# Kernel tuning notes

Measured on AMD Instinct MI355X. Metric: run time of the kernel, lower is better.

The kernel has to match this reference:

```python
import jax, jax.numpy as jnp
import numpy as np

B, DIM, H, W = 8, 384, 64, 64
HEADS = 8
D = DIM // HEADS            # 48, per-head channel dim
DH = D // 2                 # 24
D2 = D // 3 * 2             # 32, conv_up hidden width (ratio=3)


def setup_inputs() -> dict:
    key = jax.random.key(0)
    ks = jax.random.split(key, 12)
    rn = lambda k, s, sc=0.05: jax.random.normal(k, s, dtype=jnp.float32) * sc
    return {
        "x": rn(ks[0], (B, DIM, H, W), 1.0),
        "w_qkv": rn(ks[1], (3 * DIM, DIM)),          # 1x1 conv dim->3dim, no bias
        "w_dw": rn(ks[2], (3 * DIM, 1, 3, 3)),       # depthwise 3x3, groups=3dim
        "temperature": jnp.ones((HEADS, 1, 1), jnp.float32),
        "w_ar": rn(ks[3], (1, D)),                   # conv_attn_right
        "w_vr": rn(ks[4], (DH, D)),                  # conv_v_right
        "w_up1": rn(ks[5], (D2, DH)),                # conv_up[0]
        "b_up1": jnp.zeros((D2,), jnp.float32),
        "ln_g": jnp.ones((D2, HEADS, 1), jnp.float32),   # LayerNorm([D2, 8, 1])
        "ln_b": jnp.zeros((D2, HEADS, 1), jnp.float32),
        "w_up2": rn(ks[6], (D, D2)),                 # conv_up[3]
        "b_up2": jnp.zeros((D,), jnp.float32),
        "w_al": rn(ks[7], (DH, D)),                  # conv_attn_left
        "w_vl": rn(ks[8], (DH, D)),                  # conv_v_left
        "w_proj": rn(ks[9], (DIM, HEADS)),           # project_out: Conv2d(heads, dim, 1)
    }


def reference(x, w_qkv, w_dw, temperature, w_ar, w_vr, w_up1, b_up1,
              ln_g, ln_b, w_up2, b_up2, w_al, w_vl, w_proj):
    b, c, h, w = x.shape
    hw = h * w
    # qkv = dwconv3x3(conv1x1(x)); the torch module computes this identically in
    # both spatial_pool and channel_pool, so compute once.
    qkv = jnp.einsum('oc,bchw->bohw', w_qkv, x)
    qkv = jax.lax.conv_general_dilated(
        qkv, w_dw, window_strides=(1, 1), padding='SAME',
        feature_group_count=3 * c, dimension_numbers=('NCHW', 'OIHW', 'NCHW'))
    q, k, v = jnp.split(qkv, 3, axis=1)
    hsplit = lambda t: t.reshape(b, HEADS, D, hw)        # 'b (head c) h w -> b head c (h w)'
    q, k, v = hsplit(q), hsplit(k), hsplit(v)
    l2n = lambda t: t / jnp.maximum(jnp.linalg.norm(t, axis=-1, keepdims=True), 1e-12)
    # elementwise q*k attention, temperature-scaled, softmax over spatial (hw)
    attn = jax.nn.softmax(l2n(q) * l2n(k) * temperature, axis=-1)   # [b,heads,D,hw]

    # ---- spatial_pool branch (produces channel gate) ----
    input_x = jnp.einsum('od,bhdn->bhon', w_vr, v)                  # [b,heads,DH,hw]
    cmask = jax.nn.softmax(jnp.einsum('od,bhdn->bhon', w_ar, attn), axis=-1)  # [b,heads,1,hw]
    ctx = jnp.einsum('bhin,bhjn->bhji', cmask, input_x)             # [b,heads,DH,1]
    ctx = ctx.transpose(0, 2, 1, 3)                                 # [b,DH,heads,1]
    t = jnp.einsum('op,bphl->bohl', w_up1, ctx) + b_up1[None, :, None, None]  # [b,D2,8,1]
    mu = t.mean(axis=(1, 2, 3), keepdims=True)
    var = t.var(axis=(1, 2, 3), keepdims=True)
    t = (t - mu) / jnp.sqrt(var + 1e-5) * ln_g[None] + ln_b[None]
    t = jax.nn.relu(t)
    t = jnp.einsum('op,bphl->bohl', w_up2, t) + b_up2[None, :, None, None]    # [b,D,8,1]
    # torch .view(b, head*d, 1, 1) on a [b, d, head, 1] tensor: plain reshape
    mask_ch = jax.nn.sigmoid(t).reshape(b, c, 1, 1)
    out_spatial = x * mask_ch

    # ---- channel_pool branch (produces spatial gate) ----
    g_x = jnp.einsum('od,bhdn->bhon', w_al, attn)                   # [b,heads,DH,hw]
    avg_x = jax.nn.softmax(g_x.mean(axis=-1), axis=-1)              # [b,heads,DH]
    theta_x = jnp.einsum('od,bhdn->bhon', w_vl, v)                  # [b,heads,DH,hw]
    mask_sp = jax.nn.sigmoid(jnp.einsum('bho,bhon->bhn', avg_x, theta_x))
    mask_sp = mask_sp.reshape(b, HEADS, h, w)
    mask_sp = jnp.einsum('oh,bhxy->boxy', w_proj, mask_sp)          # project_out
    out_channel = x * mask_sp

    return out_spatial + out_channel
```

## Files before the change

### kernel.cpp

```cpp
#include <hip/hip_runtime.h>
#include <math.h>
#include <stdint.h>

#define B_     8
#define DIM_   384
#define HEADS_ 8
#define D_     48
#define DH_    24
#define D2_    32
#define HW_    4096
#define IMG    64
#define CH3    1152

typedef __attribute__((ext_vector_type(8))) __bf16   bf16x8;
typedef __attribute__((ext_vector_type(4))) float    f32x4;
typedef __attribute__((ext_vector_type(8))) unsigned short u16x8;

__device__ __forceinline__ float b2f(unsigned short h){
  union { uint32_t u; float f; } v; v.u = ((uint32_t)h) << 16; return v.f;
}
__device__ __forceinline__ unsigned short f2b(float f){
  union { float f; uint32_t u; } v; v.f = f;
  uint32_t r = v.u + 0x7fffu + ((v.u >> 16) & 1u);
  return (unsigned short)(r >> 16);
}

__device__ __forceinline__ float wred_sum(float v){
#pragma unroll
  for (int m = 32; m; m >>= 1) v += __shfl_xor(v, m);
  return v;
}
__device__ __forceinline__ float wred_max(float v){
#pragma unroll
  for (int m = 32; m; m >>= 1) v = fmaxf(v, __shfl_xor(v, m));
  return v;
}
__device__ __forceinline__ float wred_min(float v){
#pragma unroll
  for (int m = 32; m; m >>= 1) v = fminf(v, __shfl_xor(v, m));
  return v;
}
template<int OP>
__device__ __forceinline__ float block_red(float v, float* lds){
  if (OP == 0) v = wred_sum(v);
  else if (OP == 1) v = wred_max(v);
  else v = wred_min(v);
  const int lane = threadIdx.x & 63;
  const int wid  = threadIdx.x >> 6;
  __syncthreads();
  if (lane == 0) lds[wid] = v;
  __syncthreads();
  const int nw = blockDim.x >> 6;
  float r = lds[0];
  for (int i = 1; i < nw; ++i){
    float o = lds[i];
    if (OP == 0) r += o; else if (OP == 1) r = fmaxf(r, o); else r = fminf(r, o);
  }
  return r;
}

__global__ __launch_bounds__(256)
void k_cvtw(const float* __restrict__ w, unsigned short* __restrict__ wb){
  const int i = (blockIdx.x * 256 + threadIdx.x) * 4;
  float4 v = *reinterpret_cast<const float4*>(w + i);
  wb[i+0] = f2b(v.x); wb[i+1] = f2b(v.y); wb[i+2] = f2b(v.z); wb[i+3] = f2b(v.w);
}

__global__ __launch_bounds__(256)
void k_prep(const float* __restrict__ x, unsigned short* __restrict__ xT){
  __shared__ unsigned short Ts[64][66];
  const int t = threadIdx.x;
  const float* xb = x + ((size_t)blockIdx.z * DIM_ + blockIdx.y * 64) * HW_ + blockIdx.x * 64;
#pragma unroll
  for (int rr = 0; rr < 4; ++rr){
    const int r = (t >> 4) + rr * 16;
    const int c = (t & 15) * 4;
    float4 v = *reinterpret_cast<const float4*>(xb + (size_t)r * HW_ + c);
    Ts[r][c+0] = f2b(v.x); Ts[r][c+1] = f2b(v.y); Ts[r][c+2] = f2b(v.z); Ts[r][c+3] = f2b(v.w);
  }
  __syncthreads();
  const int rn = t >> 2, kc = (t & 3) * 16;
  unsigned short* yb = xT + ((size_t)blockIdx.z * HW_ + blockIdx.x * 64 + rn) * DIM_
                          + blockIdx.y * 64 + kc;
  u16x8 o0, o1;
#pragma unroll
  for (int j = 0; j < 8; ++j){ o0[j] = Ts[kc + j][rn]; o1[j] = Ts[kc + 8 + j][rn]; }
  *reinterpret_cast<u16x8*>(yb)     = o0;
  *reinterpret_cast<u16x8*>(yb + 8) = o1;
}

__global__ __launch_bounds__(256, 2)
void k_gemm(const unsigned short* __restrict__ wb, const unsigned short* __restrict__ xT,
            unsigned short* __restrict__ qkv){
  const int b  = blockIdx.z;
  const int m0 = blockIdx.y * 128;
  const int n0 = blockIdx.x * 128;
  __shared__ unsigned short As[128 * 64];
  __shared__ unsigned short Bs[128 * 64];
  const int t = threadIdx.x;
  const int lane = t & 63;
  const int w = t >> 6, wr = w >> 1, wc = w & 1;
  f32x4 acc[4][4];
#pragma unroll
  for (int i = 0; i < 4; ++i)
#pragma unroll
    for (int j = 0; j < 4; ++j) acc[i][j] = (f32x4){0.f,0.f,0.f,0.f};

  const unsigned short* Ag = wb + (size_t)m0 * DIM_;
  const unsigned short* Bg = xT + ((size_t)b * HW_ + n0) * DIM_;

  for (int k0 = 0; k0 < DIM_; k0 += 64){
#pragma unroll
    for (int i = 0; i < 4; ++i){
      const int q = i * 256 + t;
      const int qb = q & ~63;
      const int r = q >> 3, c = q & 7;
      __builtin_amdgcn_global_load_lds(
        (const __attribute__((address_space(1))) void*)(Ag + (size_t)r * DIM_ + k0 + c * 8),
        (__attribute__((address_space(3))) void*)(As + qb * 8), 16, 0, 0);
    }
#pragma unroll
    for (int i = 0; i < 4; ++i){
      const int q = i * 256 + t;
      const int qb = q & ~63;
      const int r = q >> 3, c = q & 7;
      __builtin_amdgcn_global_load_lds(
        (const __attribute__((address_space(1))) void*)(Bg + (size_t)r * DIM_ + k0 + c * 8),
        (__attribute__((address_space(3))) void*)(Bs + qb * 8), 16, 0, 0);
    }
    __syncthreads();
#pragma unroll
    for (int ks = 0; ks < 2; ++ks){
      const int kb = ks * 32 + (lane >> 4) * 8;
      bf16x8 af[4], bfr[4];
#pragma unroll
      for (int mi = 0; mi < 4; ++mi){
        const int row = wr * 64 + mi * 16 + (lane & 15);
        af[mi] = *reinterpret_cast<const bf16x8*>(As + row * 64 + kb);
      }
#pragma unroll
      for (int ni = 0; ni < 4; ++ni){
        const int row = wc * 64 + ni * 16 + (lane & 15);
        bfr[ni] = *reinterpret_cast<const bf16x8*>(Bs + row * 64 + kb);
      }
#pragma unroll
      for (int mi = 0; mi < 4; ++mi)
#pragma unroll
        for (int ni = 0; ni < 4; ++ni)
          acc[mi][ni] = __builtin_amdgcn_mfma_f32_16x16x32_bf16(af[mi], bfr[ni], acc[mi][ni], 0, 0, 0);
    }
    __syncthreads();
  }
  unsigned short* yb = qkv + ((size_t)b * CH3 + m0) * HW_ + n0;
#pragma unroll
  for (int mi = 0; mi < 4; ++mi){
    const int rbase = wr * 64 + mi * 16 + (lane >> 4) * 4;
#pragma unroll
    for (int ni = 0; ni < 4; ++ni){
      const int col = wc * 64 + ni * 16 + (lane & 15);
#pragma unroll
      for (int r = 0; r < 4; ++r)
        yb[(size_t)(rbase + r) * HW_ + col] = f2b(acc[mi][ni][r]);
    }
  }
}

__global__ __launch_bounds__(256)
void k_dwconv(unsigned short* __restrict__ qkv, const float* __restrict__ w_dw){
  const int pc = blockIdx.x;
  const int ch = pc % CH3;
  unsigned short* plane = qkv + (size_t)pc * HW_;
  const int t  = threadIdx.x;
  const int y  = t >> 2;
  const int x0 = (t & 3) * 16;
  float w9[9];
#pragma unroll
  for (int i = 0; i < 9; ++i) w9[i] = w_dw[ch * 9 + i];
  float acc16[16];
#pragma unroll
  for (int j = 0; j < 16; ++j) acc16[j] = 0.f;
#pragma unroll
  for (int dy = -1; dy <= 1; ++dy){
    const int yy = y + dy;
    if ((unsigned)yy >= (unsigned)IMG) continue;
    const unsigned short* rp = plane + yy * IMG;
    u16x8 C0 = *reinterpret_cast<const u16x8*>(rp + x0);
    u16x8 C1 = *reinterpret_cast<const u16x8*>(rp + x0 + 8);
    float rw[18];
    rw[0]  = (x0 > 0)  ? b2f(rp[x0 - 1])  : 0.f;
    rw[17] = (x0 < 48) ? b2f(rp[x0 + 16]) : 0.f;
#pragma unroll
    for (int j = 0; j < 8; ++j){ rw[1+j] = b2f(C0[j]); rw[9+j] = b2f(C1[j]); }
    const float w0 = w9[(dy+1)*3], w1 = w9[(dy+1)*3+1], w2 = w9[(dy+1)*3+2];
#pragma unroll
    for (int j = 0; j < 16; ++j)
      acc16[j] = fmaf(rw[j], w0, fmaf(rw[j+1], w1, fmaf(rw[j+2], w2, acc16[j])));
  }
  __syncthreads();
  u16x8 o0, o1;
#pragma unroll
  for (int j = 0; j < 8; ++j){ o0[j] = f2b(acc16[j]); o1[j] = f2b(acc16[8+j]); }
  *reinterpret_cast<u16x8*>(plane + (size_t)y * IMG + x0)     = o0;
  *reinterpret_cast<u16x8*>(plane + (size_t)y * IMG + x0 + 8) = o1;
}

__global__ __launch_bounds__(256)
void k_rowstats(const unsigned short* __restrict__ dqkv, const float* __restrict__ temperature,
                const float* __restrict__ w_ar, float* __restrict__ prm){
  const int bid  = blockIdx.x;
  const int d    = bid % D_;
  const int head = (bid / D_) % HEADS_;
  const int b    = bid / (D_ * HEADS_);
  const int cq   = head * D_ + d;
  const unsigned short* qp = dqkv + ((size_t)b * CH3 + cq) * HW_;
  const unsigned short* kp = qp + (size_t)DIM_ * HW_;
  __shared__ float lds[8];
  const int t = threadIdx.x;
  float p[16];
  float sq = 0.f, sk = 0.f, pmx = -3.0e38f, pmn = 3.0e38f;
  {
    u16x8 q0 = *reinterpret_cast<const u16x8*>(qp + t * 16);
    u16x8 q1 = *reinterpret_cast<const u16x8*>(qp + t * 16 + 8);
    u16x8 k0 = *reinterpret_cast<const u16x8*>(kp + t * 16);
    u16x8 k1 = *reinterpret_cast<const u16x8*>(kp + t * 16 + 8);
#pragma unroll
    for (int j = 0; j < 8; ++j){
      float fq = b2f(q0[j]), fk = b2f(k0[j]);
      sq = fmaf(fq, fq, sq); sk = fmaf(fk, fk, sk);
      p[j] = fq * fk; pmx = fmaxf(pmx, p[j]); pmn = fminf(pmn, p[j]);
    }
#pragma unroll
    for (int j = 0; j < 8; ++j){
      float fq = b2f(q1[j]), fk = b2f(k1[j]);
      sq = fmaf(fq, fq, sq); sk = fmaf(fk, fk, sk);
      p[8+j] = fq * fk; pmx = fmaxf(pmx, p[8+j]); pmn = fminf(pmn, p[8+j]);
    }
  }
  sq  = block_red<0>(sq, lds);
  sk  = block_red<0>(sk, lds);
  pmx = block_red<1>(pmx, lds);
  pmn = block_red<2>(pmn, lds);
  const float nq = fmaxf(sqrtf(sq), 1e-12f);
  const float nk = fmaxf(sqrtf(sk), 1e-12f);
  const float c  = temperature[head] / (nq * nk);
  const float m  = (c >= 0.f) ? c * pmx : c * pmn;
  float se = 0.f;
#pragma unroll
  for (int j = 0; j < 16; ++j) se += expf(fmaf(c, p[j], -m));
  se = block_red<0>(se, lds);
  if (t == 0){
    prm[bid*3+0] = c;
    prm[bid*3+1] = m;
    prm[bid*3+2] = w_ar[d] / se;
  }
}

__global__ __launch_bounds__(256)
void k_attn_a(const unsigned short* __restrict__ dqkv, const float* __restrict__ prm,
              float* __restrict__ abuf){
  const int bh   = blockIdx.y;
  const int head = bh & 7, b = bh >> 3;
  const int t = threadIdx.x;
  const int px0 = (blockIdx.x * 256 + t) * 2;
  __shared__ float pc[D_ * 3];
  for (int i = t; i < D_ * 3; i += 256) pc[i] = prm[bh * (D_ * 3) + i];
  __syncthreads();
  const unsigned short* qb = dqkv + ((size_t)b * CH3 + head * D_) * HW_ + px0;
  const unsigned short* kb = qb + (size_t)DIM_ * HW_;
  float a0 = 0.f, a1 = 0.f;
  for (int d = 0; d < D_; ++d){
    const uint32_t qv = *reinterpret_cast<const uint32_t*>(qb + (size_t)d * HW_);
    const uint32_t kv = *reinterpret_cast<const uint32_t*>(kb + (size_t)d * HW_);
    const float cc = pc[d*3], mm = pc[d*3+1], ww = pc[d*3+2];
    const float p0 = b2f((unsigned short)qv) * b2f((unsigned short)kv);
    const float p1 = b2f((unsigned short)(qv >> 16)) * b2f((unsigned short)(kv >> 16));
    a0 = fmaf(ww, expf(fmaf(cc, p0, -mm)), a0);
    a1 = fmaf(ww, expf(fmaf(cc, p1, -mm)), a1);
  }
  float2 o; o.x = a0; o.y = a1;
  *reinterpret_cast<float2*>(abuf + (size_t)bh * HW_ + px0) = o;
}

__global__ __launch_bounds__(256)
void k_cmask(float* __restrict__ abuf){
  const int bh = blockIdx.x;
  float* a = abuf + (size_t)bh * HW_;
  __shared__ float lds[8];
  const int t = threadIdx.x;
  float va[16];
  float mx = -3.0e38f;
#pragma unroll
  for (int i = 0; i < 16; ++i){ va[i] = a[t + i*256]; mx = fmaxf(mx, va[i]); }
  mx = block_red<1>(mx, lds);
  float s = 0.f;
#pragma unroll
  for (int i = 0; i < 16; ++i){ va[i] = expf(va[i]-mx); s += va[i]; }
  s = block_red<0>(s, lds);
  const float inv = 1.f / s;
#pragma unroll
  for (int i = 0; i < 16; ++i) a[t + i*256] = va[i]*inv;
}

__global__ __launch_bounds__(256)
void k_vctx(const unsigned short* __restrict__ dqkv, const float* __restrict__ abuf,
            float* __restrict__ vctx){
  const int bid  = blockIdx.x;
  const int d    = bid % D_;
  const int head = (bid / D_) % HEADS_;
  const int b    = bid / (D_ * HEADS_);
  const unsigned short* vp = dqkv + ((size_t)b * CH3 + 2*DIM_ + head*D_ + d) * HW_;
  const float* cm = abuf + ((size_t)(b * HEADS_ + head)) * HW_;
  __shared__ float lds[8];
  const int t = threadIdx.x;
  float s = 0.f;
  u16x8 v0 = *reinterpret_cast<const u16x8*>(vp + t * 16);
  u16x8 v1 = *reinterpret_cast<const u16x8*>(vp + t * 16 + 8);
#pragma unroll
  for (int j = 0; j < 8; ++j) s = fmaf(cm[t*16 + j],     b2f(v0[j]), s);
#pragma unroll
  for (int j = 0; j < 8; ++j) s = fmaf(cm[t*16 + 8 + j], b2f(v1[j]), s);
  s = block_red<0>(s, lds);
  if (t == 0) vctx[bid] = s;
}

__global__ __launch_bounds__(256)
void k_spmask(const unsigned short* __restrict__ dqkv, const float* __restrict__ w_al,
              const float* __restrict__ w_vl, float* __restrict__ spb){
  const int bh   = blockIdx.y;
  const int head = bh & 7, b = bh >> 3;
  const int t = threadIdx.x;
  const int px0 = (blockIdx.x * 256 + t) * 2;
  __shared__ float u[D_];
  __shared__ float avg[DH_];
  if (t < DH_){
    float s = 0.f;
    for (int d = 0; d < D_; ++d) s += w_al[t*D_ + d];
    avg[t] = s * (1.f/(float)HW_);
  }
  __syncthreads();
  if (t == 0){
    float mx = avg[0];
    for (int o = 1; o < DH_; ++o) mx = fmaxf(mx, avg[o]);
    float s = 0.f;
    for (int o = 0; o < DH_; ++o){ avg[o] = expf(avg[o]-mx); s += avg[o]; }
    const float inv = 1.f/s;
    for (int o = 0; o < DH_; ++o) avg[o] *= inv;
  }
  __syncthreads();
  if (t < D_){
    float s = 0.f;
    for (int o = 0; o < DH_; ++o) s = fmaf(avg[o], w_vl[o*D_ + t], s);
    u[t] = s;
  }
  __syncthreads();
  const unsigned short* vb = dqkv + ((size_t)b * CH3 + 2*DIM_ + head*D_) * HW_ + px0;
  float a0 = 0.f, a1 = 0.f;
  for (int d = 0; d < D_; ++d){
    const uint32_t vv = *reinterpret_cast<const uint32_t*>(vb + (size_t)d * HW_);
    const float ud = u[d];
    a0 = fmaf(ud, b2f((unsigned short)vv), a0);
    a1 = fmaf(ud, b2f((unsigned short)(vv >> 16)), a1);
  }
  float2 o;
  o.x = 1.f/(1.f + expf(-a0));
  o.y = 1.f/(1.f + expf(-a1));
  *reinterpret_cast<float2*>(spb + (size_t)bh * HW_ + px0) = o;
}

__global__ __launch_bounds__(256)
void k_maskch(const float* __restrict__ vctx, const float* __restrict__ w_vr,
              const float* __restrict__ w_up1, const float* __restrict__ b_up1,
              const float* __restrict__ ln_g, const float* __restrict__ ln_b,
              const float* __restrict__ w_up2, const float* __restrict__ b_up2,
              float* __restrict__ mch){
  const int b = blockIdx.x;
  const int t = threadIdx.x;
  __shared__ float vc[HEADS_*D_];
  __shared__ float cx[HEADS_*DH_];
  __shared__ float t1[D2_*HEADS_];
  __shared__ float lds[8];
  for (int i = t; i < HEADS_*D_; i += 256) vc[i] = vctx[b*HEADS_*D_ + i];
  __syncthreads();
  if (t < HEADS_*DH_){
    const int head = t / DH_, o = t % DH_;
    float s = 0.f;
    for (int d = 0; d < D_; ++d) s = fmaf(w_vr[o*D_+d], vc[head*D_+d], s);
    cx[head*DH_+o] = s;
  }
  __syncthreads();
  const int o2 = t >> 3, hh = t & 7;
  float val = b_up1[o2];
  for (int o = 0; o < DH_; ++o) val = fmaf(w_up1[o2*DH_+o], cx[hh*DH_+o], val);
  const float mu  = block_red<0>(val, lds) * (1.f/256.f);
  const float dv  = val - mu;
  const float var = block_red<0>(dv*dv, lds) * (1.f/256.f);
  float yv = dv / sqrtf(var + 1e-5f);
  yv = fmaf(yv, ln_g[t], ln_b[t]);
  yv = fmaxf(yv, 0.f);
  t1[t] = yv;
  __syncthreads();
  for (int idx = t; idx < D_*HEADS_; idx += 256){
    const int d = idx >> 3, head2 = idx & 7;
    float s = b_up2[d];
    for (int o = 0; o < D2_; ++o) s = fmaf(w_up2[d*D2_+o], t1[o*HEADS_+head2], s);
    mch[b*DIM_ + idx] = 1.f/(1.f + expf(-s));
  }
}

__global__ __launch_bounds__(256)
void k_out(const float* __restrict__ x, const float* __restrict__ spb,
           const float* __restrict__ mch, const float* __restrict__ w_proj,
           float* __restrict__ out){
  const int b  = blockIdx.z;
  const int c0 = blockIdx.y * 16;
  const int n  = blockIdx.x * 1024 + threadIdx.x * 4;
  float4 sv[8];
#pragma unroll
  for (int h = 0; h < 8; ++h)
    sv[h] = *reinterpret_cast<const float4*>(spb + ((size_t)(b*8+h))*HW_ + n);
  for (int ci = 0; ci < 16; ++ci){
    const int c = c0 + ci;
    const float g = mch[b*DIM_ + c];
    float4 gv; gv.x = g; gv.y = g; gv.z = g; gv.w = g;
#pragma unroll
    for (int h = 0; h < 8; ++h){
      const float wp = w_proj[c*8+h];
      gv.x = fmaf(wp, sv[h].x, gv.x); gv.y = fmaf(wp, sv[h].y, gv.y);
      gv.z = fmaf(wp, sv[h].z, gv.z); gv.w = fmaf(wp, sv[h].w, gv.w);
    }
    const size_t off = ((size_t)b*DIM_ + c)*HW_ + n;
    float4 xv = *reinterpret_cast<const float4*>(x + off);
    xv.x *= gv.x; xv.y *= gv.y; xv.z *= gv.z; xv.w *= gv.w;
    *reinterpret_cast<float4*>(out + off) = xv;
  }
}

extern "C" void kernel_launch(void* const* d_in, const int* in_sizes, int n_in,
                              void* d_out, int out_size, void* d_ws, size_t ws_size,
                              hipStream_t stream) {
  const float* x      = (const float*)d_in[0];
  const float* w_qkv  = (const float*)d_in[1];
  const float* w_dw   = (const float*)d_in[2];
  const float* temp   = (const float*)d_in[3];
  const float* w_ar   = (const float*)d_in[4];
  const float* w_vr   = (const float*)d_in[5];
  const float* w_up1  = (const float*)d_in[6];
  const float* b_up1  = (const float*)d_in[7];
  const float* ln_g   = (const float*)d_in[8];
  const float* ln_b   = (const float*)d_in[9];
  const float* w_up2  = (const float*)d_in[10];
  const float* b_up2  = (const float*)d_in[11];
  const float* w_al   = (const float*)d_in[12];
  const float* w_vl   = (const float*)d_in[13];
  const float* w_proj = (const float*)d_in[14];
  float* out = (float*)d_out;

  unsigned short* qkvb = (unsigned short*)d_ws;
  unsigned short* xT   = qkvb + (size_t)B_*CH3*HW_;
  unsigned short* wb   = xT + (size_t)B_*HW_*DIM_;
  float* prm  = (float*)(wb + (size_t)CH3*DIM_);
  float* abuf = prm + 3*B_*HEADS_*D_;
  float* vctx = abuf + (size_t)B_*HEADS_*HW_;
  float* spb  = vctx + B_*HEADS_*D_;
  float* mch  = spb + (size_t)B_*HEADS_*HW_;

  k_cvtw<<<dim3((CH3*DIM_)/1024), 256, 0, stream>>>(w_qkv, wb);
  k_prep<<<dim3(HW_/64, DIM_/64, B_), 256, 0, stream>>>(x, xT);
  k_gemm<<<dim3(HW_/128, CH3/128, B_), 256, 0, stream>>>(wb, xT, qkvb);
  k_dwconv<<<dim3(B_*CH3), 256, 0, stream>>>(qkvb, w_dw);
  k_rowstats<<<dim3(B_*HEADS_*D_), 256, 0, stream>>>(qkvb, temp, w_ar, prm);
  k_attn_a<<<dim3(8, B_*HEADS_), 256, 0, stream>>>(qkvb, prm, abuf);
  k_cmask<<<dim3(B_*HEADS_), 256, 0, stream>>>(abuf);
  k_vctx<<<dim3(B_*HEADS_*D_), 256, 0, stream>>>(qkvb, abuf, vctx);
  k_spmask<<<dim3(8, B_*HEADS_), 256, 0, stream>>>(qkvb, w_al, w_vl, spb);
  k_maskch<<<dim3(B_), 256, 0, stream>>>(vctx, w_vr, w_up1, b_up1, ln_g, ln_b,
                                         w_up2, b_up2, mch);
  k_out<<<dim3(HW_/1024, DIM_/16, B_), 256, 0, stream>>>(x, spb, mch, w_proj, out);
}
```

Before: 265.4 us.

## Double-buffer and swizzle GEMM LDS; fuse q/k depthwise conv with row stats

```diff
diff --git a/kernel.cpp b/kernel.cpp
--- a/kernel.cpp
+++ b/kernel.cpp
@@ -59,124 +59,8 @@
   return r;
 }
 
-__global__ __launch_bounds__(256)
-void k_cvtw(const float* __restrict__ w, unsigned short* __restrict__ wb){
-  const int i = (blockIdx.x * 256 + threadIdx.x) * 4;
-  float4 v = *reinterpret_cast<const float4*>(w + i);
-  wb[i+0] = f2b(v.x); wb[i+1] = f2b(v.y); wb[i+2] = f2b(v.z); wb[i+3] = f2b(v.w);
-}
-
-__global__ __launch_bounds__(256)
-void k_prep(const float* __restrict__ x, unsigned short* __restrict__ xT){
-  __shared__ unsigned short Ts[64][66];
-  const int t = threadIdx.x;
-  const float* xb = x + ((size_t)blockIdx.z * DIM_ + blockIdx.y * 64) * HW_ + blockIdx.x * 64;
-#pragma unroll
-  for (int rr = 0; rr < 4; ++rr){
-    const int r = (t >> 4) + rr * 16;
-    const int c = (t & 15) * 4;
-    float4 v = *reinterpret_cast<const float4*>(xb + (size_t)r * HW_ + c);
-    Ts[r][c+0] = f2b(v.x); Ts[r][c+1] = f2b(v.y); Ts[r][c+2] = f2b(v.z); Ts[r][c+3] = f2b(v.w);
-  }
-  __syncthreads();
-  const int rn = t >> 2, kc = (t & 3) * 16;
-  unsigned short* yb = xT + ((size_t)blockIdx.z * HW_ + blockIdx.x * 64 + rn) * DIM_
-                          + blockIdx.y * 64 + kc;
-  u16x8 o0, o1;
-#pragma unroll
-  for (int j = 0; j < 8; ++j){ o0[j] = Ts[kc + j][rn]; o1[j] = Ts[kc + 8 + j][rn]; }
-  *reinterpret_cast<u16x8*>(yb)     = o0;
-  *reinterpret_cast<u16x8*>(yb + 8) = o1;
-}
-
-__global__ __launch_bounds__(256, 2)
-void k_gemm(const unsigned short* __restrict__ wb, const unsigned short* __restrict__ xT,
-            unsigned short* __restrict__ qkv){
-  const int b  = blockIdx.z;
-  const int m0 = blockIdx.y * 128;
-  const int n0 = blockIdx.x * 128;
-  __shared__ unsigned short As[128 * 64];
-  __shared__ unsigned short Bs[128 * 64];
-  const int t = threadIdx.x;
-  const int lane = t & 63;
-  const int w = t >> 6, wr = w >> 1, wc = w & 1;
-  f32x4 acc[4][4];
-#pragma unroll
-  for (int i = 0; i < 4; ++i)
-#pragma unroll
-    for (int j = 0; j < 4; ++j) acc[i][j] = (f32x4){0.f,0.f,0.f,0.f};
-
-  const unsigned short* Ag = wb + (size_t)m0 * DIM_;
-  const unsigned short* Bg = xT + ((size_t)b * HW_ + n0) * DIM_;
-
-  for (int k0 = 0; k0 < DIM_; k0 += 64){
-#pragma unroll
-    for (int i = 0; i < 4; ++i){
-      const int q = i * 256 + t;
-      const int qb = q & ~63;
-      const int r = q >> 3, c = q & 7;
-      __builtin_amdgcn_global_load_lds(
-        (const __attribute__((address_space(1))) void*)(Ag + (size_t)r * DIM_ + k0 + c * 8),
-        (__attribute__((address_space(3))) void*)(As + qb * 8), 16, 0, 0);
-    }
-#pragma unroll
-    for (int i = 0; i < 4; ++i){
-      const int q = i * 256 + t;
-      const int qb = q & ~63;
-      const int r = q >> 3, c = q & 7;
-      __builtin_amdgcn_global_load_lds(
-        (const __attribute__((address_space(1))) void*)(Bg + (size_t)r * DIM_ + k0 + c * 8),
-        (__attribute__((address_space(3))) void*)(Bs + qb * 8), 16, 0, 0);
-    }
-    __syncthreads();
-#pragma unroll
-    for (int ks = 0; ks < 2; ++ks){
-      const int kb = ks * 32 + (lane >> 4) * 8;
-      bf16x8 af[4], bfr[4];
-#pragma unroll
-      for (int mi = 0; mi < 4; ++mi){
-        const int row = wr * 64 + mi * 16 + (lane & 15);
-        af[mi] = *reinterpret_cast<const bf16x8*>(As + row * 64 + kb);
-      }
-#pragma unroll
-      for (int ni = 0; ni < 4; ++ni){
-        const int row = wc * 64 + ni * 16 + (lane & 15);
-        bfr[ni] = *reinterpret_cast<const bf16x8*>(Bs + row * 64 + kb);
-      }
-#pragma unroll
-      for (int mi = 0; mi < 4; ++mi)
-#pragma unroll
-        for (int ni = 0; ni < 4; ++ni)
-          acc[mi][ni] = __builtin_amdgcn_mfma_f32_16x16x32_bf16(af[mi], bfr[ni], acc[mi][ni], 0, 0, 0);
-    }
-    __syncthreads();
-  }
-  unsigned short* yb = qkv + ((size_t)b * CH3 + m0) * HW_ + n0;
-#pragma unroll
-  for (int mi = 0; mi < 4; ++mi){
-    const int rbase = wr * 64 + mi * 16 + (lane >> 4) * 4;
-#pragma unroll
-    for (int ni = 0; ni < 4; ++ni){
-      const int col = wc * 64 + ni * 16 + (lane & 15);
-#pragma unroll
-      for (int r = 0; r < 4; ++r)
-        yb[(size_t)(rbase + r) * HW_ + col] = f2b(acc[mi][ni][r]);
-    }
-  }
-}
-
-__global__ __launch_bounds__(256)
-void k_dwconv(unsigned short* __restrict__ qkv, const float* __restrict__ w_dw){
-  const int pc = blockIdx.x;
-  const int ch = pc % CH3;
-  unsigned short* plane = qkv + (size_t)pc * HW_;
-  const int t  = threadIdx.x;
-  const int y  = t >> 2;
-  const int x0 = (t & 3) * 16;
-  float w9[9];
-#pragma unroll
-  for (int i = 0; i < 9; ++i) w9[i] = w_dw[ch * 9 + i];
-  float acc16[16];
+__device__ __forceinline__ void dwplane16(const unsigned short* __restrict__ plane,
+                                          const float* w9, int y, int x0, float* acc16){
 #pragma unroll
   for (int j = 0; j < 16; ++j) acc16[j] = 0.f;
 #pragma unroll
@@ -196,45 +80,163 @@
     for (int j = 0; j < 16; ++j)
       acc16[j] = fmaf(rw[j], w0, fmaf(rw[j+1], w1, fmaf(rw[j+2], w2, acc16[j])));
   }
-  __syncthreads();
+}
+
+__global__ __launch_bounds__(256)
+void k_cvtw(const float* __restrict__ w, unsigned short* __restrict__ wb){
+  const int i = (blockIdx.x * 256 + threadIdx.x) * 4;
+  float4 v = *reinterpret_cast<const float4*>(w + i);
+  wb[i+0] = f2b(v.x); wb[i+1] = f2b(v.y); wb[i+2] = f2b(v.z); wb[i+3] = f2b(v.w);
+}
+
+__global__ __launch_bounds__(256)
+void k_prep(const float* __restrict__ x, unsigned short* __restrict__ xT){
+  __shared__ unsigned short Ts[64][66];
+  const int t = threadIdx.x;
+  const float* xb = x + ((size_t)blockIdx.z * DIM_ + blockIdx.y * 64) * HW_ + blockIdx.x * 64;
+#pragma unroll
+  for (int rr = 0; rr < 4; ++rr){
+    const int r = (t >> 4) + rr * 16;
+    const int c = (t & 15) * 4;
+    float4 v = *reinterpret_cast<const float4*>(xb + (size_t)r * HW_ + c);
+    Ts[r][c+0] = f2b(v.x); Ts[r][c+1] = f2b(v.y); Ts[r][c+2] = f2b(v.z); Ts[r][c+3] = f2b(v.w);
+  }
+  __syncthreads();
+  const int rn = t >> 2, kc = (t & 3) * 16;
+  unsigned short* yb = xT + ((size_t)blockIdx.z * HW_ + blockIdx.x * 64 + rn) * DIM_
+                          + blockIdx.y * 64 + kc;
   u16x8 o0, o1;
 #pragma unroll
-  for (int j = 0; j < 8; ++j){ o0[j] = f2b(acc16[j]); o1[j] = f2b(acc16[8+j]); }
-  *reinterpret_cast<u16x8*>(plane + (size_t)y * IMG + x0)     = o0;
-  *reinterpret_cast<u16x8*>(plane + (size_t)y * IMG + x0 + 8) = o1;
-}
-
-__global__ __launch_bounds__(256)
-void k_rowstats(const unsigned short* __restrict__ dqkv, const float* __restrict__ temperature,
-                const float* __restrict__ w_ar, float* __restrict__ prm){
-  const int bid  = blockIdx.x;
-  const int d    = bid % D_;
-  const int head = (bid / D_) % HEADS_;
-  const int b    = bid / (D_ * HEADS_);
-  const int cq   = head * D_ + d;
-  const unsigned short* qp = dqkv + ((size_t)b * CH3 + cq) * HW_;
-  const unsigned short* kp = qp + (size_t)DIM_ * HW_;
+  for (int j = 0; j < 8; ++j){ o0[j] = Ts[kc + j][rn]; o1[j] = Ts[kc + 8 + j][rn]; }
+  *reinterpret_cast<u16x8*>(yb)     = o0;
+  *reinterpret_cast<u16x8*>(yb + 8) = o1;
+}
+
+__global__ __launch_bounds__(256)
+void k_gemm(const unsigned short* __restrict__ wb, const unsigned short* __restrict__ xT,
+            unsigned short* __restrict__ qkv){
+  const int b  = blockIdx.z;
+  const int m0 = blockIdx.y * 128;
+  const int n0 = blockIdx.x * 128;
+  __shared__ unsigned short As[2][128 * 64];
+  __shared__ unsigned short Bs[2][128 * 64];
+  const int t = threadIdx.x;
+  const int lane = t & 63;
+  const int fr = lane & 15;
+  const int ld = lane >> 4;
+  const int w = t >> 6, wr = w >> 1, wc = w & 1;
+  f32x4 acc[4][4];
+#pragma unroll
+  for (int i = 0; i < 4; ++i)
+#pragma unroll
+    for (int j = 0; j < 4; ++j) acc[i][j] = (f32x4){0.f,0.f,0.f,0.f};
+
+  const unsigned short* Ag = wb + (size_t)m0 * DIM_;
+  const unsigned short* Bg = xT + ((size_t)b * HW_ + n0) * DIM_;
+
+  auto stage = [&](int buf, int k0){
+#pragma unroll
+    for (int i = 0; i < 4; ++i){
+      const int q = i * 256 + t;
+      const int qb = q & ~63;
+      const int r = q >> 3, c = q & 7;
+      const int cs = c ^ (r & 7);
+      __builtin_amdgcn_global_load_lds(
+        (const __attribute__((address_space(1))) void*)(Ag + (size_t)r * DIM_ + k0 + cs * 8),
+        (__attribute__((address_space(3))) void*)(&As[buf][qb * 8]), 16, 0, 0);
+    }
+#pragma unroll
+    for (int i = 0; i < 4; ++i){
+      const int q = i * 256 + t;
+      const int qb = q & ~63;
+      const int r = q >> 3, c = q & 7;
+      const int cs = c ^ (r & 7);
+      __builtin_amdgcn_global_load_lds(
+        (const __attribute__((address_space(1))) void*)(Bg + (size_t)r * DIM_ + k0 + cs * 8),
+        (__attribute__((address_space(3))) void*)(&Bs[buf][qb * 8]), 16, 0, 0);
+    }
+  };
+
+  stage(0, 0);
+  for (int it = 0; it < 6; ++it){
+    const int cur = it & 1;
+    if (it < 5){
+      stage(cur ^ 1, (it + 1) * 64);
+      asm volatile("s_waitcnt vmcnt(8)" ::: "memory");
+    } else {
+      asm volatile("s_waitcnt vmcnt(0)" ::: "memory");
+    }
+    __builtin_amdgcn_s_barrier();
+    asm volatile("" ::: "memory");
+#pragma unroll
+    for (int ks = 0; ks < 2; ++ks){
+      bf16x8 af[4], bfr[4];
+#pragma unroll
+      for (int mi = 0; mi < 4; ++mi){
+        const int row = wr * 64 + mi * 16 + fr;
+        const int cc = (ks * 4 + ld) ^ (row & 7);
+        af[mi] = *reinterpret_cast<const bf16x8*>(&As[cur][row * 64 + cc * 8]);
+      }
+#pragma unroll
+      for (int ni = 0; ni < 4; ++ni){
+        const int row = wc * 64 + ni * 16 + fr;
+        const int cc = (ks * 4 + ld) ^ (row & 7);
+        bfr[ni] = *reinterpret_cast<const bf16x8*>(&Bs[cur][row * 64 + cc * 8]);
+      }
+#pragma unroll
+      for (int mi = 0; mi < 4; ++mi)
+#pragma unroll
+        for (int ni = 0; ni < 4; ++ni)
+          acc[mi][ni] = __builtin_amdgcn_mfma_f32_16x16x32_bf16(af[mi], bfr[ni], acc[mi][ni], 0, 0, 0);
+    }
+    asm volatile("" ::: "memory");
+    __builtin_amdgcn_s_barrier();
+  }
+  unsigned short* yb = qkv + ((size_t)b * CH3 + m0) * HW_ + n0;
+#pragma unroll
+  for (int mi = 0; mi < 4; ++mi){
+    const int rbase = wr * 64 + mi * 16 + (lane >> 4) * 4;
+#pragma unroll
+    for (int ni = 0; ni < 4; ++ni){
+      const int col = wc * 64 + ni * 16 + (lane & 15);
+#pragma unroll
+      for (int r = 0; r < 4; ++r)
+        yb[(size_t)(rbase + r) * HW_ + col] = f2b(acc[mi][ni][r]);
+    }
+  }
+}
+
+__global__ __launch_bounds__(256)
+void k_dwqk(unsigned short* __restrict__ qkv, const float* __restrict__ w_dw,
+            const float* __restrict__ temperature, const float* __restrict__ w_ar,
+            float* __restrict__ prm){
+  const int pc = blockIdx.x;
+  const int ch = pc % DIM_;
+  const int b  = pc / DIM_;
+  const int d  = ch % D_;
+  const int head = ch / D_;
+  unsigned short* qp = qkv + ((size_t)b * CH3 + ch) * HW_;
+  unsigned short* kp = qp + (size_t)DIM_ * HW_;
+  const int t  = threadIdx.x;
+  const int y  = t >> 2;
+  const int x0 = (t & 3) * 16;
+  float wq9[9], wk9[9];
+#pragma unroll
+  for (int i = 0; i < 9; ++i){ wq9[i] = w_dw[ch*9+i]; wk9[i] = w_dw[(DIM_+ch)*9+i]; }
+  float aq[16], ak[16];
+  dwplane16(qp, wq9, y, x0, aq);
+  dwplane16(kp, wk9, y, x0, ak);
+  unsigned short qs[16], kss[16];
+#pragma unroll
+  for (int j = 0; j < 16; ++j){ qs[j] = f2b(aq[j]); kss[j] = f2b(ak[j]); }
   __shared__ float lds[8];
-  const int t = threadIdx.x;
   float p[16];
   float sq = 0.f, sk = 0.f, pmx = -3.0e38f, pmn = 3.0e38f;
-  {
-    u16x8 q0 = *reinterpret_cast<const u16x8*>(qp + t * 16);
-    u16x8 q1 = *reinterpret_cast<const u16x8*>(qp + t * 16 + 8);
-    u16x8 k0 = *reinterpret_cast<const u16x8*>(kp + t * 16);
-    u16x8 k1 = *reinterpret_cast<const u16x8*>(kp + t * 16 + 8);
-#pragma unroll
-    for (int j = 0; j < 8; ++j){
-      float fq = b2f(q0[j]), fk = b2f(k0[j]);
-      sq = fmaf(fq, fq, sq); sk = fmaf(fk, fk, sk);
-      p[j] = fq * fk; pmx = fmaxf(pmx, p[j]); pmn = fminf(pmn, p[j]);
-    }
-#pragma unroll
-    for (int j = 0; j < 8; ++j){
-      float fq = b2f(q1[j]), fk = b2f(k1[j]);
-      sq = fmaf(fq, fq, sq); sk = fmaf(fk, fk, sk);
-      p[8+j] = fq * fk; pmx = fmaxf(pmx, p[8+j]); pmn = fminf(pmn, p[8+j]);
-    }
+#pragma unroll
+  for (int j = 0; j < 16; ++j){
+    const float fq = b2f(qs[j]), fk = b2f(kss[j]);
+    sq = fmaf(fq, fq, sq); sk = fmaf(fk, fk, sk);
+    p[j] = fq * fk; pmx = fmaxf(pmx, p[j]); pmn = fminf(pmn, p[j]);
   }
   sq  = block_red<0>(sq, lds);
   sk  = block_red<0>(sk, lds);
@@ -248,11 +250,43 @@
 #pragma unroll
   for (int j = 0; j < 16; ++j) se += expf(fmaf(c, p[j], -m));
   se = block_red<0>(se, lds);
+  u16x8 o0, o1;
+#pragma unroll
+  for (int j = 0; j < 8; ++j){ o0[j] = qs[j]; o1[j] = qs[8+j]; }
+  *reinterpret_cast<u16x8*>(qp + (size_t)y * IMG + x0)     = o0;
+  *reinterpret_cast<u16x8*>(qp + (size_t)y * IMG + x0 + 8) = o1;
+#pragma unroll
+  for (int j = 0; j < 8; ++j){ o0[j] = kss[j]; o1[j] = kss[8+j]; }
+  *reinterpret_cast<u16x8*>(kp + (size_t)y * IMG + x0)     = o0;
+  *reinterpret_cast<u16x8*>(kp + (size_t)y * IMG + x0 + 8) = o1;
   if (t == 0){
-    prm[bid*3+0] = c;
-    prm[bid*3+1] = m;
-    prm[bid*3+2] = w_ar[d] / se;
-  }
+    prm[pc*3+0] = c;
+    prm[pc*3+1] = m;
+    prm[pc*3+2] = w_ar[d] / se;
+  }
+}
+
+__global__ __launch_bounds__(256)
+void k_dwv(unsigned short* __restrict__ qkv, const float* __restrict__ w_dw){
+  const int pc = blockIdx.x;
+  const int ch = pc % DIM_;
+  const int b  = pc / DIM_;
+  const int cv = 2*DIM_ + ch;
+  unsigned short* plane = qkv + ((size_t)b * CH3 + cv) * HW_;
+  const int t  = threadIdx.x;
+  const int y  = t >> 2;
+  const int x0 = (t & 3) * 16;
+  float w9[9];
+#pragma unroll
+  for (int i = 0; i < 9; ++i) w9[i] = w_dw[cv*9+i];
+  float acc16[16];
+  dwplane16(plane, w9, y, x0, acc16);
+  __syncthreads();
+  u16x8 o0, o1;
+#pragma unroll
+  for (int j = 0; j < 8; ++j){ o0[j] = f2b(acc16[j]); o1[j] = f2b(acc16[8+j]); }
+  *reinterpret_cast<u16x8*>(plane + (size_t)y * IMG + x0)     = o0;
+  *reinterpret_cast<u16x8*>(plane + (size_t)y * IMG + x0 + 8) = o1;
 }
 
 __global__ __launch_bounds__(256)
@@ -467,8 +501,8 @@
   k_cvtw<<<dim3((CH3*DIM_)/1024), 256, 0, stream>>>(w_qkv, wb);
   k_prep<<<dim3(HW_/64, DIM_/64, B_), 256, 0, stream>>>(x, xT);
   k_gemm<<<dim3(HW_/128, CH3/128, B_), 256, 0, stream>>>(wb, xT, qkvb);
-  k_dwconv<<<dim3(B_*CH3), 256, 0, stream>>>(qkvb, w_dw);
-  k_rowstats<<<dim3(B_*HEADS_*D_), 256, 0, stream>>>(qkvb, temp, w_ar, prm);
+  k_dwqk<<<dim3(B_*DIM_), 256, 0, stream>>>(qkvb, w_dw, temp, w_ar, prm);
+  k_dwv<<<dim3(B_*DIM_), 256, 0, stream>>>(qkvb, w_dw);
   k_attn_a<<<dim3(8, B_*HEADS_), 256, 0, stream>>>(qkvb, prm, abuf);
   k_cmask<<<dim3(B_*HEADS_), 256, 0, stream>>>(abuf);
   k_vctx<<<dim3(B_*HEADS_*D_), 256, 0, stream>>>(qkvb, abuf, vctx);
```

New measurement: 262.5 us. About the same (-1.1%).
